# Optimization experiments

Measured on AMD Instinct MI355X. Metric: run time of the kernel, lower is better.

Reference implementation:

```python
import jax, jax.numpy as jnp
import numpy as np

B_, L, D_MODEL = 8, 2048, 512
EXPAND, D_STATE, HEADDIM, NGROUPS, D_CONV = 2, 16, 64, 1, 4
D_INNER = EXPAND * D_MODEL            # 1024
NHEADS = D_INNER // HEADDIM           # 16
CONV_DIM = D_INNER + 2 * NGROUPS * D_STATE   # 1056
D_IN_PROJ = 2 * D_INNER + 2 * NGROUPS * D_STATE + NHEADS  # 2096
EPS = 1e-5


def _mamba_params(key):
    ks = jax.random.split(key, 5)
    in_proj_w = jax.random.normal(ks[0], (D_IN_PROJ, D_MODEL), jnp.float32) * (D_MODEL ** -0.5)
    conv_w = jax.random.normal(ks[1], (CONV_DIM, 1, D_CONV), jnp.float32) * (D_CONV ** -0.5)
    conv_b = jnp.zeros((CONV_DIM,), jnp.float32)
    # inverse-softplus of dt ~ U[1e-3, 0.1] (mamba-ssm style init)
    dt_bias = jnp.log(jnp.expm1(jax.random.uniform(ks[2], (NHEADS,), jnp.float32, 1e-3, 0.1)))
    A_log = jnp.log(jax.random.uniform(ks[3], (NHEADS,), jnp.float32, 1.0, 16.0))
    Dp = jnp.ones((NHEADS,), jnp.float32)
    norm_w = jnp.ones((D_INNER,), jnp.float32)
    out_proj_w = jax.random.normal(ks[4], (D_MODEL, D_INNER), jnp.float32) * (D_INNER ** -0.5)
    return [in_proj_w, conv_w, conv_b, dt_bias, A_log, Dp, norm_w, out_proj_w]


def setup_inputs() -> dict:
    key = jax.random.key(0)
    k0, k1, k2 = jax.random.split(key, 3)
    d = {"x": jax.random.normal(k0, (B_, L, D_MODEL), jnp.float32)}
    names = ["in_proj_w", "conv_w", "conv_b", "dt_bias", "A_log", "Dp", "norm_w", "out_proj_w"]
    for pre, k in (("fwd_", k1), ("bwd_", k2)):
        for n, p in zip(names, _mamba_params(k)):
            d[pre + n] = p
    return d


def _silu(v):
    return v * jax.nn.sigmoid(v)


def _mamba2(u, in_proj_w, conv_w, conv_b, dt_bias, A_log, Dp, norm_w, out_proj_w):
    b, l, _ = u.shape
    zxbcdt = u @ in_proj_w.T                                # (b,l,D_IN_PROJ)
    z, xBC, dt = jnp.split(zxbcdt, [D_INNER, D_INNER + CONV_DIM], axis=-1)
    # causal depthwise conv1d + silu
    xc = jnp.transpose(xBC, (0, 2, 1))                      # (b,C,l)
    xc = jax.lax.conv_general_dilated(xc, conv_w, (1,), [(D_CONV - 1, 0)],
                                      feature_group_count=CONV_DIM)
    xBC = _silu(jnp.transpose(xc, (0, 2, 1)) + conv_b)      # (b,l,C)
    xs, Bm, Cm = jnp.split(xBC, [D_INNER, D_INNER + NGROUPS * D_STATE], axis=-1)
    xs = xs.reshape(b, l, NHEADS, HEADDIM)
    Bm = Bm.reshape(b, l, NGROUPS, D_STATE)[:, :, 0]        # ngroups=1 -> (b,l,N)
    Cm = Cm.reshape(b, l, NGROUPS, D_STATE)[:, :, 0]
    dt = jax.nn.softplus(dt + dt_bias)                      # (b,l,H)
    A = -jnp.exp(A_log)                                     # (H,)
    dA = jnp.exp(dt * A)                                    # (b,l,H), in (0,1)

    def step(h, inp):
        dA_t, dt_t, x_t, B_t, C_t = inp
        h = h * dA_t[:, :, None, None] + jnp.einsum('bh,bhp,bn->bhpn', dt_t, x_t, B_t)
        y = jnp.einsum('bhpn,bn->bhp', h, C_t)
        return h, y

    h0 = jnp.zeros((b, NHEADS, HEADDIM, D_STATE), u.dtype)
    seq = (jnp.moveaxis(dA, 1, 0), jnp.moveaxis(dt, 1, 0), jnp.moveaxis(xs, 1, 0),
           jnp.moveaxis(Bm, 1, 0), jnp.moveaxis(Cm, 1, 0))
    _, ys = jax.lax.scan(step, h0, seq)
    y = jnp.moveaxis(ys, 0, 1) + xs * Dp[None, None, :, None]   # (b,l,H,P)
    y = y.reshape(b, l, D_INNER)
    # RMSNormGated (norm_before_gate=False): rmsnorm(y * silu(z)) * w
    y = y * _silu(z)
    y = y * jax.lax.rsqrt(jnp.mean(y * y, axis=-1, keepdims=True) + EPS) * norm_w
    return y @ out_proj_w.T


def reference(x,
              fwd_in_proj_w, fwd_conv_w, fwd_conv_b, fwd_dt_bias, fwd_A_log, fwd_Dp, fwd_norm_w, fwd_out_proj_w,
              bwd_in_proj_w, bwd_conv_w, bwd_conv_b, bwd_dt_bias, bwd_A_log, bwd_Dp, bwd_norm_w, bwd_out_proj_w):
    fwd = _mamba2(x, fwd_in_proj_w, fwd_conv_w, fwd_conv_b, fwd_dt_bias, fwd_A_log, fwd_Dp, fwd_norm_w, fwd_out_proj_w)
    bwd = _mamba2(x[:, ::-1], bwd_in_proj_w, bwd_conv_w, bwd_conv_b, bwd_dt_bias, bwd_A_log, bwd_Dp, bwd_norm_w, bwd_out_proj_w)
    return fwd + bwd[:, ::-1]
```

## Files before the change

### kernel.cpp

```cpp
#include <hip/hip_runtime.h>
#include <stdint.h>

#define L_SEQ   2048
#define BATCH   8
#define DMODEL  512
#define DINNER  1024
#define NHEADS  16
#define HEADDIM 64
#define DSTATE  16
#define CONVDIM 1056
#define DINPROJ 2096
#define NPROJ   4192
#define NPROJ_P 4224
#define NROWS   (BATCH*L_SEQ)
#define NCH     32
#define CHLEN   64
#define XBCW    1072

typedef __attribute__((ext_vector_type(8))) short short8;
typedef __attribute__((ext_vector_type(4))) float f32x4;

static __device__ __forceinline__ unsigned short f2bf(float f) {
    unsigned int u = __float_as_uint(f);
    u += 0x7FFF + ((u >> 16) & 1);
    return (unsigned short)(u >> 16);
}
static __device__ __forceinline__ float bf2f(unsigned short u) {
    return __uint_as_float((unsigned int)u << 16);
}
static __device__ __forceinline__ float silu(float v) {
    return v / (1.f + __expf(-v));
}
static __device__ __forceinline__ void glds16(const unsigned short* g, unsigned short* l) {
    __builtin_amdgcn_global_load_lds(
        (const __attribute__((address_space(1))) unsigned int*)g,
        (__attribute__((address_space(3))) unsigned int*)l, 16, 0, 0);
}

#define PREP_N1 (NROWS*DMODEL)
#define PREP_N2 (NPROJ_P*DMODEL)
#define PREP_N3 (512*2048)
#define PREP_T  ((PREP_N1+PREP_N2+PREP_N3)/4)
static __device__ __forceinline__ uint2 pack4(float4 v) {
    uint2 o;
    o.x = (unsigned int)f2bf(v.x) | ((unsigned int)f2bf(v.y) << 16);
    o.y = (unsigned int)f2bf(v.z) | ((unsigned int)f2bf(v.w) << 16);
    return o;
}
__global__ void k_prep(const float* __restrict__ x,
                       const float* __restrict__ fwi, const float* __restrict__ bwi,
                       const float* __restrict__ fow, const float* __restrict__ bow,
                       unsigned short* __restrict__ XB, unsigned short* __restrict__ W1,
                       unsigned short* __restrict__ W2) {
    int i = blockIdx.x * 256 + threadIdx.x;
    if (i >= PREP_T) return;
    int j4 = i * 4;
    if (j4 < PREP_N1) {
        *(uint2*)&XB[j4] = pack4(*(const float4*)&x[j4]);
    } else if (j4 < PREP_N1 + PREP_N2) {
        int j = j4 - PREP_N1;
        const int FS = DINPROJ * DMODEL;
        uint2 o = {0u, 0u};
        if (j < 2 * FS)
            o = pack4(j < FS ? *(const float4*)&fwi[j] : *(const float4*)&bwi[j - FS]);
        *(uint2*)&W1[j] = o;
    } else {
        int j = j4 - PREP_N1 - PREP_N2;
        int n = j >> 11, k = j & 2047;
        const float* s = (k < DINNER) ? &fow[n * DINNER + k] : &bow[n * DINNER + k - DINNER];
        *(uint2*)&W2[j] = pack4(*(const float4*)s);
    }
}

#define BM 128
#define BN 128
#define BK 32

#define GEMM_BODY(NROUNDS, EPILOGUE)                                                        \
    __shared__ __align__(16) unsigned short as[2][BM][BK];                                  \
    __shared__ __align__(16) unsigned short bs[2][BN][BK];                                  \
    const int tid = threadIdx.x;                                                            \
    const int lane = tid & 63;                                                              \
    const int wave = tid >> 6;                                                              \
    const int wm = (wave & 1) * 64;                                                         \
    const int wn = (wave >> 1) * 64;                                                        \
    const int l16 = lane & 15;                                                              \
    const int q = lane >> 4;                                                                \
    const int sr = wave * 32;                                                               \
    const int lr = lane >> 2;                                                               \
    const int lc = (lane & 3) * 8;                                                          \
    f32x4 acc[4][4];                                                                        \
    for (int i = 0; i < 4; i++)                                                             \
        for (int j = 0; j < 4; j++) acc[i][j] = (f32x4){0.f, 0.f, 0.f, 0.f};                \
    const unsigned short* Ab = A + (size_t)(bm + sr + lr) * K + koff + lc;                  \
    const unsigned short* Bb = Bw + (size_t)(bn + sr + lr) * K + koff + lc;                 \
    glds16(Ab, &as[0][sr][0]);                                                              \
    glds16(Ab + (size_t)16 * K, &as[0][sr + 16][0]);                                        \
    glds16(Bb, &bs[0][sr][0]);                                                              \
    glds16(Bb + (size_t)16 * K, &bs[0][sr + 16][0]);                                        \
    __syncthreads();                                                                        \
    for (int r = 0; r < NROUNDS; r++) {                                                     \
        const int pb = r & 1;                                                               \
        if (r + 1 < NROUNDS) {               \
            const int kb = (r + 1) * BK;                                                    \
            glds16(Ab + kb, &as[pb ^ 1][sr][0]);                                            \
            glds16(Ab + (size_t)16 * K + kb, &as[pb ^ 1][sr + 16][0]);                      \
            glds16(Bb + kb, &bs[pb ^ 1][sr][0]);                                            \
            glds16(Bb + (size_t)16 * K + kb, &bs[pb ^ 1][sr + 16][0]);                      \
        }                                                                                   \
        short8 af[4], bfr[4];                                                               \
        for (int i = 0; i < 4; i++) af[i] = *(const short8*)&as[pb][wm + i * 16 + l16][q * 8]; \
        for (int j = 0; j < 4; j++) bfr[j] = *(const short8*)&bs[pb][wn + j * 16 + l16][q * 8]; \
        for (int i = 0; i < 4; i++)                                                         \
            for (int j = 0; j < 4; j++)                                                     \
                acc[i][j] = __builtin_amdgcn_mfma_f32_16x16x32_bf16(af[i], bfr[j], acc[i][j], 0, 0, 0); \
        __syncthreads();                          \
    }                                                                                       \
    EPILOGUE

__global__ __launch_bounds__(256, 4) void k_gemm_proj(const unsigned short* __restrict__ A,
                                                      const unsigned short* __restrict__ Bw,
                                                      unsigned short* __restrict__ ZG,
                                                      unsigned short* __restrict__ XBCDT) {
    const int K = DMODEL;
    const int N = NPROJ;
    const int lin = blockIdx.x;
    const int xcd = lin & 7;
    const int idx = lin >> 3;
    const int mloc = idx & 15;
    const int n_tile = idx >> 4;
    const int bm = (mloc * 8 + xcd) * BM;
    const int bn = n_tile * BN;
    const int koff = 0;
    GEMM_BODY(16, {
        for (int i = 0; i < 4; i++) {
            int row0 = bm + wm + i * 16 + q * 4;
            for (int j = 0; j < 4; j++) {
                int col = bn + wn + j * 16 + l16;
                if (col < N) {
                    int dir = col >= DINPROJ;
                    int cc = col - dir * DINPROJ;
                    for (int r = 0; r < 4; r++) {
                        unsigned short v = f2bf(acc[i][j][r]);
                        size_t rowo = (size_t)(dir * NROWS + row0 + r);
                        if (cc < DINNER)
                            ZG[rowo * DINNER + cc] = v;
                        else
                            XBCDT[rowo * XBCW + (cc - DINNER)] = v;
                    }
                }
            }
        }
    })
}

__global__ __launch_bounds__(256, 4) void k_gemm_out(const unsigned short* __restrict__ A,
                                                     const unsigned short* __restrict__ Bw,
                                                     float* __restrict__ C) {
    const int K = 2048;
    const int lin = blockIdx.x;
    const int xcd = lin & 7;
    const int idx = lin >> 3;
    const int mloc = idx & 15;
    const int n_tile = idx >> 4;
    const int bm = (mloc * 8 + xcd) * BM;
    const int bn = n_tile * BN;
    const int koff = 0;
    GEMM_BODY(64, {
        for (int i = 0; i < 4; i++) {
            int row0 = bm + wm + i * 16 + q * 4;
            for (int j = 0; j < 4; j++) {
                int col = bn + wn + j * 16 + l16;
                for (int r = 0; r < 4; r++)
                    C[(size_t)(row0 + r) * 512 + col] = acc[i][j][r];
            }
        }
    })
}

__global__ __launch_bounds__(256) void k_conv2(const unsigned short* __restrict__ XBCDT,
                                               const float* __restrict__ fw_w, const float* __restrict__ fw_b,
                                               const float* __restrict__ bw_w, const float* __restrict__ bw_b,
                                               unsigned short* __restrict__ XS, float* __restrict__ BCb) {
    __shared__ unsigned short sm[70][256];
    int t = threadIdx.x;
    int bidx = blockIdx.x;
    int lcn = bidx & 31;
    int b   = (bidx >> 5) & 7;
    int dir = (bidx >> 8) & 1;
    int ct  = bidx >> 9;
    int c0 = ct * 256;
    int l0 = lcn * 64;
    int c = c0 + t;
    const unsigned short* src = XBCDT + (size_t)dir * NROWS * XBCW;
    {
        const int rr = t >> 5;
        const int ch = t & 31;
        const int cc0 = c0 + ch * 8;
        const bool cok16 = (cc0 + 8 <= XBCW);
        const short8 z8 = {0, 0, 0, 0, 0, 0, 0, 0};
#pragma unroll
        for (int pass = 0; pass < 9; ++pass) {
            int r = pass * 8 + rr;
            if (r < 70) {
                int li = l0 - 3 + r;
                short8 v = z8;
                if (li >= 0 && li < L_SEQ && cok16)
                    v = *(const short8*)&src[(size_t)((b << 11) + li) * XBCW + cc0];
                *(short8*)&sm[r][ch * 8] = v;
            }
        }
    }
    __syncthreads();
    if (c >= CONVDIM) return;
    const float* w = (dir ? bw_w : fw_w) + c * 4;
    float bias = (dir ? bw_b : fw_b)[c];
    float wr[4];
    if (dir) { wr[0] = w[3]; wr[1] = w[2]; wr[2] = w[1]; wr[3] = w[0]; }
    else     { wr[0] = w[0]; wr[1] = w[1]; wr[2] = w[2]; wr[3] = w[3]; }
    int o = dir ? 3 : 0;
    float w0 = bf2f(sm[o][t]), w1 = bf2f(sm[o + 1][t]), w2 = bf2f(sm[o + 2][t]);
    unsigned short* xso = XS + (size_t)dir * NROWS * DINNER;
    float* bco = BCb + (size_t)dir * NROWS * 32;
    int rowbase = (b << 11) + l0;
#pragma unroll 4
    for (int l = 0; l < 64; l++) {
        float w3 = bf2f(sm[l + o + 3][t]);
        float acc = ((wr[0] * w0 + wr[1] * w1) + (wr[2] * w2 + wr[3] * w3)) + bias;
        float v = silu(acc);
        int row = rowbase + l;
        if (c < DINNER)
            xso[(size_t)row * DINNER + c] = f2bf(v);
        else
            bco[(size_t)row * 32 + (c - DINNER)] = v;
        w0 = w1; w1 = w2; w2 = w3;
    }
}

__global__ void k_dt(const unsigned short* __restrict__ XBCDT,
                     const float* __restrict__ fdtb, const float* __restrict__ fAl,
                     const float* __restrict__ bdtb, const float* __restrict__ bAl,
                     float* __restrict__ DT, float* __restrict__ DA) {
    int gid = blockIdx.x * 256 + threadIdx.x;
    if (gid >= 2 * NROWS * NHEADS) return;
    int h = gid & 15;
    int row = (gid >> 4) & (NROWS - 1);
    int dir = gid >> 18;
    float dtb = (dir ? bdtb : fdtb)[h];
    float Al = (dir ? bAl : fAl)[h];
    float x = bf2f(XBCDT[(size_t)(dir * NROWS + row) * XBCW + CONVDIM + h]) + dtb;
    float dt = (x > 15.f) ? x : log1pf(__expf(x));
    float dA = __expf(-__expf(Al) * dt);
    DT[gid] = dt;
    DA[gid] = dA;
}

__global__ __launch_bounds__(64) void k_scan_state(const unsigned short* __restrict__ XS,
                                                   const float* __restrict__ BCb,
                                                   const float* __restrict__ DT,
                                                   const float* __restrict__ DA,
                                                   float* __restrict__ S, float* __restrict__ P) {
    int idx = blockIdx.x;
    int c = idx & 31, hp = (idx >> 5) & 7, b = (idx >> 8) & 7, dir = idx >> 11;
    int t = threadIdx.x;
    int h = hp * 2 + (t >> 5);
    int p0 = (t & 31) * 2;
    const unsigned short* xs = XS + (size_t)dir * NROWS * DINNER;
    const float* bc = BCb + (size_t)dir * NROWS * 32;
    const float* dtp = DT + (size_t)dir * NROWS * NHEADS;
    const float* dap = DA + (size_t)dir * NROWS * NHEADS;
    float hreg0[16], hreg1[16];
#pragma unroll
    for (int n = 0; n < 16; n++) { hreg0[n] = 0.f; hreg1[n] = 0.f; }
    float Pp = 1.f;
#pragma unroll 4
    for (int tl = 0; tl < CHLEN; ++tl) {
        int tt = c * CHLEN + tl;
        int l = dir ? (L_SEQ - 1 - tt) : tt;
        int row = (b << 11) + l;
        unsigned int xv2 = *(const unsigned int*)&xs[(size_t)row * DINNER + h * HEADDIM + p0];
        float xv0 = bf2f((unsigned short)(xv2 & 0xffff));
        float xv1 = bf2f((unsigned short)(xv2 >> 16));
        float dt = dtp[row * 16 + h];
        float dA = dap[row * 16 + h];
        f32x4 Bv[4];
#pragma unroll
        for (int qq = 0; qq < 4; qq++) Bv[qq] = *(const f32x4*)&bc[(size_t)row * 32 + qq * 4];
        float k0 = dt * xv0, k1 = dt * xv1;
#pragma unroll
        for (int n = 0; n < 16; n++) {
            float bv = Bv[n >> 2][n & 3];
            hreg0[n] = fmaf(hreg0[n], dA, k0 * bv);
            hreg1[n] = fmaf(hreg1[n], dA, k1 * bv);
        }
        Pp *= dA;
    }
    int sh = (((dir * 8 + b) * 16 + h) * NCH + c);
#pragma unroll
    for (int qq = 0; qq < 4; qq++) {
        f32x4 v0 = {hreg0[qq * 4], hreg0[qq * 4 + 1], hreg0[qq * 4 + 2], hreg0[qq * 4 + 3]};
        f32x4 v1 = {hreg1[qq * 4], hreg1[qq * 4 + 1], hreg1[qq * 4 + 2], hreg1[qq * 4 + 3]};
        *(f32x4*)&S[(size_t)sh * 1024 + p0 * 16 + qq * 4] = v0;
        *(f32x4*)&S[(size_t)sh * 1024 + (p0 + 1) * 16 + qq * 4] = v1;
    }
    if ((t & 31) == 0) P[sh] = Pp;
}

__global__ void k_combine(float* __restrict__ S, const float* __restrict__ P) {
    int gid = blockIdx.x * 256 + threadIdx.x;
    if (gid >= 2 * 8 * 16 * 1024) return;
    int pn = gid & 1023;
    int base = gid >> 10;
    float H = 0.f;
#pragma unroll 4
    for (int c = 0; c < NCH; c++) {
        size_t o = ((size_t)base * NCH + c) * 1024 + pn;
        float s = S[o];
        S[o] = H;
        H = H * P[base * NCH + c] + s;
    }
}

__global__ __launch_bounds__(64) void k_scan_out(const unsigned short* __restrict__ XS,
                                                 const float* __restrict__ BCb,
                                                 const float* __restrict__ DT,
                                                 const float* __restrict__ DA,
                                                 const float* __restrict__ Hinit,
                                                 const float* __restrict__ fDp,
                                                 const float* __restrict__ bDp,
                                                 unsigned short* __restrict__ Y) {
    int idx = blockIdx.x;
    int c = idx & 31, hp = (idx >> 5) & 7, b = (idx >> 8) & 7, dir = idx >> 11;
    int t = threadIdx.x;
    int h = hp * 2 + (t >> 5);
    int p0 = (t & 31) * 2;
    const unsigned short* xs = XS + (size_t)dir * NROWS * DINNER;
    const float* bc = BCb + (size_t)dir * NROWS * 32;
    const float* dtp = DT + (size_t)dir * NROWS * NHEADS;
    const float* dap = DA + (size_t)dir * NROWS * NHEADS;
    unsigned short* yo = Y + (size_t)dir * NROWS * DINNER;
    float Dpv = (dir ? bDp : fDp)[h];
    int sh = (((dir * 8 + b) * 16 + h) * NCH + c);
    float hreg0[16], hreg1[16];
#pragma unroll
    for (int qq = 0; qq < 4; qq++) {
        f32x4 v0 = *(const f32x4*)&Hinit[(size_t)sh * 1024 + p0 * 16 + qq * 4];
        f32x4 v1 = *(const f32x4*)&Hinit[(size_t)sh * 1024 + (p0 + 1) * 16 + qq * 4];
#pragma unroll
        for (int e = 0; e < 4; e++) { hreg0[qq * 4 + e] = v0[e]; hreg1[qq * 4 + e] = v1[e]; }
    }
#pragma unroll 4
    for (int tl = 0; tl < CHLEN; ++tl) {
        int tt = c * CHLEN + tl;
        int l = dir ? (L_SEQ - 1 - tt) : tt;
        int row = (b << 11) + l;
        unsigned int xv2 = *(const unsigned int*)&xs[(size_t)row * DINNER + h * HEADDIM + p0];
        float xv0 = bf2f((unsigned short)(xv2 & 0xffff));
        float xv1 = bf2f((unsigned short)(xv2 >> 16));
        float dt = dtp[row * 16 + h];
        float dA = dap[row * 16 + h];
        f32x4 Bv[4], Cv[4];
#pragma unroll
        for (int qq = 0; qq < 4; qq++) Bv[qq] = *(const f32x4*)&bc[(size_t)row * 32 + qq * 4];
#pragma unroll
        for (int qq = 0; qq < 4; qq++) Cv[qq] = *(const f32x4*)&bc[(size_t)row * 32 + 16 + qq * 4];
        float k0 = dt * xv0, k1 = dt * xv1;
        float y0 = 0.f, y1 = 0.f;
#pragma unroll
        for (int n = 0; n < 16; n++) {
            float bv = Bv[n >> 2][n & 3];
            float cv = Cv[n >> 2][n & 3];
            hreg0[n] = fmaf(hreg0[n], dA, k0 * bv);
            hreg1[n] = fmaf(hreg1[n], dA, k1 * bv);
            y0 = fmaf(hreg0[n], cv, y0);
            y1 = fmaf(hreg1[n], cv, y1);
        }
        unsigned int yw = (unsigned int)f2bf(y0 + xv0 * Dpv)
                        | ((unsigned int)f2bf(y1 + xv1 * Dpv) << 16);
        *(unsigned int*)&yo[(size_t)row * DINNER + h * HEADDIM + p0] = yw;
    }
}

__global__ __launch_bounds__(256) void k_gatenorm(const unsigned short* __restrict__ Y,
                                                  const unsigned short* __restrict__ ZG,
                                                  const float* __restrict__ fnw,
                                                  const float* __restrict__ bnw,
                                                  unsigned short* __restrict__ NRM) {
    int bid = blockIdx.x;
    int t = threadIdx.x;
    int sub = t >> 7;
    int tt = t & 127;
    int rid = bid * 2 + sub;
    int dir = rid >> 14;
    int row = rid & (NROWS - 1);
    int c = tt * 8;
    const size_t base = (size_t)(dir * NROWS + row) * DINNER + c;
    uint4 yu = *(const uint4*)&Y[base];
    uint4 zu = *(const uint4*)&ZG[base];
    float v[8];
    {
        const unsigned int yw[4] = {yu.x, yu.y, yu.z, yu.w};
        const unsigned int zw[4] = {zu.x, zu.y, zu.z, zu.w};
#pragma unroll
        for (int e = 0; e < 4; e++) {
            v[e * 2]     = bf2f((unsigned short)(yw[e] & 0xffff)) * silu(bf2f((unsigned short)(zw[e] & 0xffff)));
            v[e * 2 + 1] = bf2f((unsigned short)(yw[e] >> 16))    * silu(bf2f((unsigned short)(zw[e] >> 16)));
        }
    }
    float ss = 0.f;
#pragma unroll
    for (int e = 0; e < 8; e++) ss += v[e] * v[e];
#pragma unroll
    for (int off = 32; off > 0; off >>= 1) ss += __shfl_down(ss, off);
    __shared__ float red[4];
    if ((t & 63) == 0) red[t >> 6] = ss;
    __syncthreads();
    float tot = red[sub * 2] + red[sub * 2 + 1];
    float scale = rsqrtf(tot * (1.f / 1024.f) + 1e-5f);
    const float* nw = (dir ? bnw : fnw) + c;
    f32x4 nw0 = *(const f32x4*)&nw[0];
    f32x4 nw1 = *(const f32x4*)&nw[4];
    unsigned int ow[4];
#pragma unroll
    for (int e = 0; e < 4; e++) {
        float a = v[e * 2]     * scale * (e < 2 ? nw0[e * 2]     : nw1[(e - 2) * 2]);
        float b = v[e * 2 + 1] * scale * (e < 2 ? nw0[e * 2 + 1] : nw1[(e - 2) * 2 + 1]);
        ow[e] = (unsigned int)f2bf(a) | ((unsigned int)f2bf(b) << 16);
    }
    uint4 o = {ow[0], ow[1], ow[2], ow[3]};
    *(uint4*)&NRM[(size_t)row * 2048 + dir * DINNER + c] = o;
}

extern "C" void kernel_launch(void* const* d_in, const int* in_sizes, int n_in,
                              void* d_out, int out_size, void* d_ws, size_t ws_size,
                              hipStream_t stream) {
    const float* x     = (const float*)d_in[0];
    const float* f_inw = (const float*)d_in[1];
    const float* f_cw  = (const float*)d_in[2];
    const float* f_cb  = (const float*)d_in[3];
    const float* f_dtb = (const float*)d_in[4];
    const float* f_Al  = (const float*)d_in[5];
    const float* f_Dp  = (const float*)d_in[6];
    const float* f_nw  = (const float*)d_in[7];
    const float* f_ow  = (const float*)d_in[8];
    const float* b_inw = (const float*)d_in[9];
    const float* b_cw  = (const float*)d_in[10];
    const float* b_cb  = (const float*)d_in[11];
    const float* b_dtb = (const float*)d_in[12];
    const float* b_Al  = (const float*)d_in[13];
    const float* b_Dp  = (const float*)d_in[14];
    const float* b_nw  = (const float*)d_in[15];
    const float* b_ow  = (const float*)d_in[16];

    char* ws = (char*)d_ws;
    size_t off = 0;
    auto alloc = [&](size_t bytes) {
        void* p = ws + off;
        off += (bytes + 255) & ~(size_t)255;
        return p;
    };
    unsigned short* XBCDT = (unsigned short*)alloc((size_t)2 * NROWS * XBCW * 2);
    unsigned short* NRM   = XBCDT;
    float* S = (float*)XBCDT;
    float* P = (float*)((char*)XBCDT + (size_t)2 * 8 * 16 * NCH * 1024 * 4);
    unsigned short* XS    = (unsigned short*)alloc((size_t)2 * NROWS * DINNER * 2);
    unsigned short* Yb    = XS;
    unsigned short* ZG    = (unsigned short*)alloc((size_t)2 * NROWS * DINNER * 2);
    unsigned short* W2    = (unsigned short*)alloc((size_t)512 * 2048 * 2);
    float* BCb  = (float*)alloc((size_t)2 * NROWS * 32 * 4);
    float* DT   = (float*)alloc((size_t)2 * NROWS * NHEADS * 4);
    float* DA   = (float*)alloc((size_t)2 * NROWS * NHEADS * 4);
    char* unionBase = (char*)alloc((size_t)16777216 + (size_t)NPROJ_P * DMODEL * 2);
    unsigned short* XB = (unsigned short*)unionBase;
    unsigned short* W1 = (unsigned short*)(unionBase + 16777216);

    if (ws_size < off) return;

    k_prep<<<(PREP_T + 255) / 256, 256, 0, stream>>>(x, f_inw, b_inw, f_ow, b_ow, XB, W1, W2);
    k_gemm_proj<<<8 * 16 * 33, 256, 0, stream>>>(XB, W1, ZG, XBCDT);
    k_conv2<<<5 * 2 * 8 * 32, 256, 0, stream>>>(XBCDT, f_cw, f_cb, b_cw, b_cb, XS, BCb);
    {
        int n = 2 * NROWS * NHEADS;
        k_dt<<<(n + 255) / 256, 256, 0, stream>>>(XBCDT, f_dtb, f_Al, b_dtb, b_Al, DT, DA);
    }
    k_scan_state<<<2 * 8 * 8 * NCH, 64, 0, stream>>>(XS, BCb, DT, DA, S, P);
    {
        int n = 2 * 8 * 16 * 1024;
        k_combine<<<(n + 255) / 256, 256, 0, stream>>>(S, P);
    }
    k_scan_out<<<2 * 8 * 8 * NCH, 64, 0, stream>>>(XS, BCb, DT, DA, S, f_Dp, b_Dp, Yb);
    k_gatenorm<<<NROWS, 256, 0, stream>>>(Yb, ZG, f_nw, b_nw, NRM);
    k_gemm_out<<<8 * 16 * 4, 256, 0, stream>>>(NRM, W2, (float*)d_out);
}
```

Measured before the change: 459.2 us.

## Triple-buffer input projection GEMM with explicit vmcnt waits and raw barriers

Rewrites the in_proj GEMM kernel from a double-buffered loop into a three-stage LDS pipeline. Loads for two k-steps ahead are issued, and explicit s_waitcnt vmcnt counts plus raw s_barrier calls replace __syncthreads. The MFMA block is wrapped in s_setprio to favour math waves. The aim is to hide global-to-LDS latency better; the cost is 50% more LDS per block, which may reduce occupancy, and correctness now depends on the hand-counted waits.

```diff
diff --git a/kernel.cpp b/kernel.cpp
--- a/kernel.cpp
+++ b/kernel.cpp
@@ -36,6 +36,9 @@
         (const __attribute__((address_space(1))) unsigned int*)g,
         (__attribute__((address_space(3))) unsigned int*)l, 16, 0, 0);
 }
+#define BARX() do { asm volatile("" ::: "memory"); __builtin_amdgcn_s_barrier(); \
+                    asm volatile("" ::: "memory"); } while (0)
+#define WAITV(n) asm volatile("s_waitcnt vmcnt(" #n ")" ::: "memory")
 
 #define PREP_N1 (NROWS*DMODEL)
 #define PREP_N2 (NPROJ_P*DMODEL)
@@ -75,6 +78,92 @@
 #define BM 128
 #define BN 128
 #define BK 32
+
+__global__ __launch_bounds__(256, 4) void k_gemm_proj(const unsigned short* __restrict__ A,
+                                                      const unsigned short* __restrict__ Bw,
+                                                      unsigned short* __restrict__ ZG,
+                                                      unsigned short* __restrict__ XBCDT) {
+    __shared__ __align__(16) unsigned short as[3][BM][BK];
+    __shared__ __align__(16) unsigned short bs[3][BN][BK];
+    const int K = DMODEL;
+    const int N = NPROJ;
+    const int lin = blockIdx.x;
+    const int xcd = lin & 7;
+    const int idx = lin >> 3;
+    const int mloc = idx & 15;
+    const int n_tile = idx >> 4;
+    const int bm = (mloc * 8 + xcd) * BM;
+    const int bn = n_tile * BN;
+    const int tid = threadIdx.x;
+    const int lane = tid & 63;
+    const int wave = tid >> 6;
+    const int wm = (wave & 1) * 64;
+    const int wn = (wave >> 1) * 64;
+    const int l16 = lane & 15;
+    const int q = lane >> 4;
+    const int sr = wave * 32;
+    const int lr = lane >> 2;
+    const int lc = (lane & 3) * 8;
+    f32x4 acc[4][4];
+#pragma unroll
+    for (int i = 0; i < 4; i++)
+#pragma unroll
+        for (int j = 0; j < 4; j++) acc[i][j] = (f32x4){0.f, 0.f, 0.f, 0.f};
+    const unsigned short* Ab = A + (size_t)(bm + sr + lr) * K + lc;
+    const unsigned short* Bb = Bw + (size_t)(bn + sr + lr) * K + lc;
+    auto STAGE = [&](int t) {
+        const int s = t % 3;
+        const int kb = t * BK;
+        glds16(Ab + kb, &as[s][sr][0]);
+        glds16(Ab + (size_t)16 * K + kb, &as[s][sr + 16][0]);
+        glds16(Bb + kb, &bs[s][sr][0]);
+        glds16(Bb + (size_t)16 * K + kb, &bs[s][sr + 16][0]);
+    };
+    STAGE(0);
+    STAGE(1);
+    for (int r = 0; r < 16; ++r) {
+        if (r) BARX();
+        if (r + 2 < 16) STAGE(r + 2);
+        if (r + 2 < 16)      WAITV(8);
+        else if (r + 1 < 16) WAITV(4);
+        else                 WAITV(0);
+        BARX();
+        const int pb = r % 3;
+        short8 af[4], bfr[4];
+#pragma unroll
+        for (int i = 0; i < 4; i++) af[i] = *(const short8*)&as[pb][wm + i * 16 + l16][q * 8];
+#pragma unroll
+        for (int j = 0; j < 4; j++) bfr[j] = *(const short8*)&bs[pb][wn + j * 16 + l16][q * 8];
+        __builtin_amdgcn_s_setprio(1);
+#pragma unroll
+        for (int i = 0; i < 4; i++)
+#pragma unroll
+            for (int j = 0; j < 4; j++)
+                acc[i][j] = __builtin_amdgcn_mfma_f32_16x16x32_bf16(af[i], bfr[j], acc[i][j], 0, 0, 0);
+        __builtin_amdgcn_s_setprio(0);
+    }
+#pragma unroll
+    for (int i = 0; i < 4; i++) {
+        int row0 = bm + wm + i * 16 + q * 4;
+#pragma unroll
+        for (int j = 0; j < 4; j++) {
+            int col = bn + wn + j * 16 + l16;
+            if (col < N) {
+                int dir = col >= DINPROJ;
+                int cc = col - dir * DINPROJ;
+#pragma unroll
+                for (int r = 0; r < 4; r++) {
+                    unsigned short v = f2bf(acc[i][j][r]);
+                    size_t rowo = (size_t)(dir * NROWS + row0 + r);
+                    if (cc < DINNER)
+                        ZG[rowo * DINNER + cc] = v;
+                    else
+                        XBCDT[rowo * XBCW + (cc - DINNER)] = v;
+                }
+            }
+        }
+    }
+}
 
 #define GEMM_BODY(NROUNDS, EPILOGUE)                                                        \
     __shared__ __align__(16) unsigned short as[2][BM][BK];                                  \
@@ -118,42 +207,6 @@
     }                                                                                       \
     EPILOGUE
 
-__global__ __launch_bounds__(256, 4) void k_gemm_proj(const unsigned short* __restrict__ A,
-                                                      const unsigned short* __restrict__ Bw,
-                                                      unsigned short* __restrict__ ZG,
-                                                      unsigned short* __restrict__ XBCDT) {
-    const int K = DMODEL;
-    const int N = NPROJ;
-    const int lin = blockIdx.x;
-    const int xcd = lin & 7;
-    const int idx = lin >> 3;
-    const int mloc = idx & 15;
-    const int n_tile = idx >> 4;
-    const int bm = (mloc * 8 + xcd) * BM;
-    const int bn = n_tile * BN;
-    const int koff = 0;
-    GEMM_BODY(16, {
-        for (int i = 0; i < 4; i++) {
-            int row0 = bm + wm + i * 16 + q * 4;
-            for (int j = 0; j < 4; j++) {
-                int col = bn + wn + j * 16 + l16;
-                if (col < N) {
-                    int dir = col >= DINPROJ;
-                    int cc = col - dir * DINPROJ;
-                    for (int r = 0; r < 4; r++) {
-                        unsigned short v = f2bf(acc[i][j][r]);
-                        size_t rowo = (size_t)(dir * NROWS + row0 + r);
-                        if (cc < DINNER)
-                            ZG[rowo * DINNER + cc] = v;
-                        else
-                            XBCDT[rowo * XBCW + (cc - DINNER)] = v;
-                    }
-                }
-            }
-        }
-    })
-}
-
 __global__ __launch_bounds__(256, 4) void k_gemm_out(const unsigned short* __restrict__ A,
                                                      const unsigned short* __restrict__ Bw,
                                                      float* __restrict__ C) {
```

Result: no change. 458.4 us (-0.2%).
